# Performance work log

Hardware: AMD Instinct MI355X
Metric: run time of the kernel (lower is better)

Reference implementation:

```python
import jax, jax.numpy as jnp
import numpy as np

A = 4096      # alleles
RPA = 20      # mean reads per allele
R = A * RPA   # total reads per data source
C = 12        # input channels (pileup features)
L = 32        # read window length
D = 32        # hidden feature dim
NOUT = 2


def setup_inputs() -> dict:
    key = jax.random.key(0)
    k = jax.random.split(key, 8)
    # ragged read counts per allele (alternating 16/24, mean 20, sums to R)
    counts0 = np.tile(np.array([16, 24], dtype=np.int64), A // 2)
    counts1 = np.tile(np.array([24, 16], dtype=np.int64), A // 2)
    return {
        "tensors0": jax.random.normal(k[0], (R, C, L), dtype=jnp.float32),
        "tensors1": jax.random.normal(k[1], (R, C, L), dtype=jnp.float32),
        "W0": jax.random.normal(k[2], (D, C), dtype=jnp.float32) * 0.1,
        "b0": jnp.zeros((D,), dtype=jnp.float32),
        "W1": jax.random.normal(k[3], (D, C), dtype=jnp.float32) * 0.1,
        "b1": jnp.zeros((D,), dtype=jnp.float32),
        "W2": jax.random.normal(k[4], (NOUT, 2 * D), dtype=jnp.float32) * 0.1,
        "b2": jnp.zeros((NOUT,), dtype=jnp.float32),
        "numReadsPerAllele0": jnp.asarray(counts0),
        "numReadsPerAllele1": jnp.asarray(counts1),
        "numAllelesPerSite": jnp.full((A // 2,), 2, dtype=jnp.int64),
        "depthMultiplier0": jnp.asarray(counts0, dtype=jnp.float32),
        "depthMultiplier1": jnp.asarray(counts1, dtype=jnp.float32),
    }


def _frames(t, W, b):
    # pointwise read-feature extractor: [R,C,L] -> [R,D,L]
    return jax.nn.relu(jnp.einsum('rcl,dc->rdl', t, W) + b[None, :, None])


def reference(tensors0, tensors1, W0, b0, W1, b1, W2, b2,
              numReadsPerAllele0, numReadsPerAllele1,
              numAllelesPerSite, depthMultiplier0, depthMultiplier1):
    nA = numReadsPerAllele0.shape[0]
    nR = tensors0.shape[0]
    # segment ids replace torch.split + per-segment torch.sum (ragged segment-sum)
    seg0 = jnp.repeat(jnp.arange(nA), numReadsPerAllele0, total_repeat_length=nR)
    seg1 = jnp.repeat(jnp.arange(nA), numReadsPerAllele1, total_repeat_length=nR)

    frames0 = _frames(tensors0, W0, b0)  # [R,D,L]
    frames1 = _frames(tensors1, W1, b1)

    red0 = jax.ops.segment_sum(frames0, seg0, num_segments=nA)  # [A,D,L]
    red1 = jax.ops.segment_sum(frames1, seg1, num_segments=nA)

    # depth normalization (normalize() in the original)
    red0 = red0 / depthMultiplier0[:, None, None]
    red1 = red1 / depthMultiplier1[:, None, None]

    reduced = jnp.concatenate((red0, red1), axis=1)  # [A, 2D, L]

    # network2 (GraphSearcher): site-specific head modeled as pool + linear
    pooled = jnp.mean(reduced, axis=2)               # [A, 2D]
    return pooled @ W2.T + b2                        # [A, NOUT]
```

## Files before the change

kernel.cpp:

```cpp
#include <hip/hip_runtime.h>

#define A_ALLELES 4096
#define CCH 12
#define LW 32
#define DH 32
#define RDF (CCH * LW)

typedef __attribute__((ext_vector_type(8)))  short bf16x8;
typedef __attribute__((ext_vector_type(16))) float f32x16;

__device__ inline unsigned pk2(float fa, float fb) {
    const unsigned a = __float_as_uint(fa), b = __float_as_uint(fb);
    return ((a + 0x8000u) >> 16) | ((b + 0x8000u) & 0xffff0000u);
}

__global__ __launch_bounds__(256) void scan_kernel(
    const int* __restrict__ c0, const int* __restrict__ c1,
    int* __restrict__ o0, int* __restrict__ o1)
{
    const int* c = (blockIdx.x == 0) ? c0 : c1;
    int*       o = (blockIdx.x == 0) ? o0 : o1;

    __shared__ int part[256];
    const int tid  = threadIdx.x;
    const int base = tid * 16;

    int loc[16];
    int s = 0;
#pragma unroll
    for (int i = 0; i < 16; ++i) { loc[i] = c[base + i]; s += loc[i]; }
    part[tid] = s;
    __syncthreads();

    for (int st = 1; st < 256; st <<= 1) {
        int v = (tid >= st) ? part[tid - st] : 0;
        __syncthreads();
        part[tid] += v;
        __syncthreads();
    }

    int excl = (tid == 0) ? 0 : part[tid - 1];
#pragma unroll
    for (int i = 0; i < 16; ++i) { o[base + i] = excl; excl += loc[i]; }
}

__global__ __launch_bounds__(256, 4) void main_kernel(
    const float* __restrict__ t0, const float* __restrict__ t1,
    const float* __restrict__ W0, const float* __restrict__ b0,
    const float* __restrict__ W1, const float* __restrict__ b1,
    const float* __restrict__ W2, const float* __restrict__ b2,
    const int*  __restrict__ cnt0, const int* __restrict__ cnt1,
    const float* __restrict__ dm0, const float* __restrict__ dm1,
    const int*  __restrict__ offs0, const int* __restrict__ offs1,
    float* __restrict__ out)
{
    __shared__ float sW2[2 * 2 * DH];
    __shared__ float sB2[2];

    const int tid = threadIdx.x;
    if (tid < 2 * 2 * DH) sW2[tid] = W2[tid];
    if (tid < 2) sB2[tid] = b2[tid];
    __syncthreads();

    const int w    = tid >> 6;
    const int lane = tid & 63;
    const int src  = blockIdx.x >> 10;
    const int a    = ((blockIdx.x & 1023) << 2) | w;

    const float* __restrict__ tens = src ? t1 : t0;
    const int*   __restrict__ cnt  = src ? cnt1 : cnt0;
    const int*   __restrict__ offs = src ? offs1 : offs0;
    const float* __restrict__ dm   = src ? dm1 : dm0;
    const float* __restrict__ gW   = src ? W1 : W0;
    const float* __restrict__ gB   = src ? b1 : b0;

    const int l = lane & 31;
    const int h = lane >> 5;

    union { bf16x8 v; unsigned u[4]; } Af;
#pragma unroll
    for (int p = 0; p < 4; ++p) {
        const int c0 = h * 8 + 2 * p, c1 = c0 + 1;
        const float f0 = (c0 < CCH) ? gW[l * CCH + c0] : 0.f;
        const float f1 = (c1 < CCH) ? gW[l * CCH + c1] : 0.f;
        Af.u[p] = pk2(f0, f1);
    }
    f32x16 cb;
#pragma unroll
    for (int reg = 0; reg < 16; ++reg)
        cb[reg] = gB[(reg & 3) + 8 * (reg >> 2) + 4 * h];

    const int n     = cnt[a];
    const int start = offs[a];
    const float* rb = tens + (size_t)start * RDF;

    const int e    = lane & 1;
    const int jj   = (lane >> 1) & 15;
    const int half = lane >> 5;
    const int q0 = 2 * ((half * 8 + e)     * 16 + jj);
    const int q1 = 2 * ((half * 8 + 2 + e) * 16 + jj);
    const int q2 = 2 * ((4 + half * 2 + e) * 16 + jj);

    float acc[16];
#pragma unroll
    for (int r = 0; r < 16; ++r) acc[r] = 0.f;

#define LOADF2(A0, A1, A2, i) do {                                    \
        const float* _p = rb + (size_t)(i) * RDF;                     \
        A0 = *reinterpret_cast<const float2*>(_p + q0);               \
        A1 = *reinterpret_cast<const float2*>(_p + q1);               \
        A2 = *reinterpret_cast<const float2*>(_p + q2); } while (0)

#define CONSUMEF2(A0, A1, A2) do {                                    \
        const float p0x = __shfl_xor(A0.x, 1, 64);                    \
        const float p0y = __shfl_xor(A0.y, 1, 64);                    \
        const float p1x = __shfl_xor(A1.x, 1, 64);                    \
        const float p1y = __shfl_xor(A1.y, 1, 64);                    \
        const float p2x = __shfl_xor(A2.x, 1, 64);                    \
        const float p2y = __shfl_xor(A2.y, 1, 64);                    \
        const float c0v = e ? p0y : A0.x;     \
        const float c1v = e ? A0.y : p0x;    \
        const float c2v = e ? p1y : A1.x;    \
        const float c3v = e ? A1.y : p1x;    \
        const float vA  = e ? p2y : A2.x;    \
        const float vB  = e ? A2.y : p2x;    \
        const float vC  = __shfl_xor(vA, 32, 64);      \
        const float vD  = __shfl_xor(vB, 32, 64);      \
        union { bf16x8 v; unsigned u[4]; } Bf;                        \
        Bf.u[0] = pk2(c0v, c1v); Bf.u[1] = pk2(c2v, c3v);             \
        Bf.u[2] = pk2(vA, vB);   Bf.u[3] = pk2(vC, vD);               \
        const f32x16 Dv = __builtin_amdgcn_mfma_f32_32x32x16_bf16(    \
            Af.v, Bf.v, cb, 0, 0, 0);                                 \
        _Pragma("unroll")                                             \
        for (int r_ = 0; r_ < 16; ++r_) acc[r_] += fmaxf(Dv[r_], 0.f); } while (0)

    const int n2 = n & ~1;
    if (n2 >= 2) {
        float2 Ra0, Ra1, Ra2, Rb0, Rb1, Rb2;
        LOADF2(Ra0, Ra1, Ra2, 0);
        LOADF2(Rb0, Rb1, Rb2, 1);
        for (int i = 0; i + 4 <= n2; i += 2) {
            CONSUMEF2(Ra0, Ra1, Ra2); LOADF2(Ra0, Ra1, Ra2, i + 2);
            CONSUMEF2(Rb0, Rb1, Rb2); LOADF2(Rb0, Rb1, Rb2, i + 3);
        }
        CONSUMEF2(Ra0, Ra1, Ra2);
        CONSUMEF2(Rb0, Rb1, Rb2);
    }
    for (int i = n2; i < n; ++i) {
        float2 T0, T1, T2;
        LOADF2(T0, T1, T2, i);
        CONSUMEF2(T0, T1, T2);
    }
#undef LOADF2
#undef CONSUMEF2

#pragma unroll
    for (int r = 0; r < 16; ++r) {
#pragma unroll
        for (int mm = 1; mm < 32; mm <<= 1)
            acc[r] += __shfl_xor(acc[r], mm, 64);
    }

    const float scale = 1.f / (32.f * dm[a]);
    float c0s = 0.f, c1s = 0.f;
#pragma unroll
    for (int r = 0; r < 16; ++r) {
        const int d = (r & 3) + 8 * (r >> 2) + 4 * h;
        const float pv = acc[r] * scale;
        c0s = fmaf(pv, sW2[0 * 2 * DH + src * DH + d], c0s);
        c1s = fmaf(pv, sW2[1 * 2 * DH + src * DH + d], c1s);
    }
    c0s += __shfl_xor(c0s, 32, 64);
    c1s += __shfl_xor(c1s, 32, 64);

    if (lane == 0) {
        if (src == 0) { c0s += sB2[0]; c1s += sB2[1]; }
        atomicAdd(&out[a * 2 + 0], c0s);
        atomicAdd(&out[a * 2 + 1], c1s);
    }
}

extern "C" void kernel_launch(void* const* d_in, const int* in_sizes, int n_in,
                              void* d_out, int out_size, void* d_ws, size_t ws_size,
                              hipStream_t stream) {
    const float* t0  = (const float*)d_in[0];
    const float* t1  = (const float*)d_in[1];
    const float* W0  = (const float*)d_in[2];
    const float* b0  = (const float*)d_in[3];
    const float* W1  = (const float*)d_in[4];
    const float* b1  = (const float*)d_in[5];
    const float* W2  = (const float*)d_in[6];
    const float* b2  = (const float*)d_in[7];
    const int*  cnt0 = (const int*)d_in[8];
    const int*  cnt1 = (const int*)d_in[9];
    const float* dm0 = (const float*)d_in[11];
    const float* dm1 = (const float*)d_in[12];

    int* offs0 = (int*)d_ws;
    int* offs1 = offs0 + A_ALLELES;

    hipMemsetAsync(d_out, 0, (size_t)out_size * sizeof(float), stream);
    scan_kernel<<<2, 256, 0, stream>>>(cnt0, cnt1, offs0, offs1);

    main_kernel<<<2048, 256, 0, stream>>>(
        t0, t1, W0, b0, W1, b1, W2, b2,
        cnt0, cnt1, dm0, dm1, offs0, offs1, (float*)d_out);
}
```

Baseline: 298.2 us.

## Process four alleles per wave with a persistent loop and deeper prefetch

Each wave now loops over four (source, allele) work items instead of handling one, so the grid shrinks from 2048 to 512 blocks. The read prefetch ring grows from two reads in flight to four, and launch bounds relax from 4 to 2 waves-per-SIMD minimum to leave room for the extra registers. The aim is more memory-level parallelism per wave and less per-block launch overhead on this bandwidth-bound read stream. The cost is lower occupancy and possible load imbalance, since 512 blocks of 4 waves may not fill all CUs evenly.

```diff
diff --git a/kernel.cpp b/kernel.cpp
--- a/kernel.cpp
+++ b/kernel.cpp
@@ -44,7 +44,7 @@
     for (int i = 0; i < 16; ++i) { o[base + i] = excl; excl += loc[i]; }
 }
 
-__global__ __launch_bounds__(256, 4) void main_kernel(
+__global__ __launch_bounds__(256, 2) void main_kernel(
     const float* __restrict__ t0, const float* __restrict__ t1,
     const float* __restrict__ W0, const float* __restrict__ b0,
     const float* __restrict__ W1, const float* __restrict__ b1,
@@ -64,35 +64,10 @@
 
     const int w    = tid >> 6;
     const int lane = tid & 63;
-    const int src  = blockIdx.x >> 10;
-    const int a    = ((blockIdx.x & 1023) << 2) | w;
-
-    const float* __restrict__ tens = src ? t1 : t0;
-    const int*   __restrict__ cnt  = src ? cnt1 : cnt0;
-    const int*   __restrict__ offs = src ? offs1 : offs0;
-    const float* __restrict__ dm   = src ? dm1 : dm0;
-    const float* __restrict__ gW   = src ? W1 : W0;
-    const float* __restrict__ gB   = src ? b1 : b0;
+    const int g    = (blockIdx.x << 2) | w;
 
     const int l = lane & 31;
     const int h = lane >> 5;
-
-    union { bf16x8 v; unsigned u[4]; } Af;
-#pragma unroll
-    for (int p = 0; p < 4; ++p) {
-        const int c0 = h * 8 + 2 * p, c1 = c0 + 1;
-        const float f0 = (c0 < CCH) ? gW[l * CCH + c0] : 0.f;
-        const float f1 = (c1 < CCH) ? gW[l * CCH + c1] : 0.f;
-        Af.u[p] = pk2(f0, f1);
-    }
-    f32x16 cb;
-#pragma unroll
-    for (int reg = 0; reg < 16; ++reg)
-        cb[reg] = gB[(reg & 3) + 8 * (reg >> 2) + 4 * h];
-
-    const int n     = cnt[a];
-    const int start = offs[a];
-    const float* rb = tens + (size_t)start * RDF;
 
     const int e    = lane & 1;
     const int jj   = (lane >> 1) & 15;
@@ -101,9 +76,38 @@
     const int q1 = 2 * ((half * 8 + 2 + e) * 16 + jj);
     const int q2 = 2 * ((4 + half * 2 + e) * 16 + jj);
 
-    float acc[16];
-#pragma unroll
-    for (int r = 0; r < 16; ++r) acc[r] = 0.f;
+#pragma unroll 1
+    for (int k = 0; k < 4; ++k) {
+        const int src = k >> 1;
+        const int a   = g + ((k & 1) << 11);
+
+        const float* __restrict__ tens = src ? t1 : t0;
+        const int*   __restrict__ cnt  = src ? cnt1 : cnt0;
+        const int*   __restrict__ offs = src ? offs1 : offs0;
+        const float* __restrict__ dm   = src ? dm1 : dm0;
+        const float* __restrict__ gW   = src ? W1 : W0;
+        const float* __restrict__ gB   = src ? b1 : b0;
+
+        union { bf16x8 v; unsigned u[4]; } Af;
+#pragma unroll
+        for (int p = 0; p < 4; ++p) {
+            const int c0 = h * 8 + 2 * p, c1 = c0 + 1;
+            const float f0 = (c0 < CCH) ? gW[l * CCH + c0] : 0.f;
+            const float f1 = (c1 < CCH) ? gW[l * CCH + c1] : 0.f;
+            Af.u[p] = pk2(f0, f1);
+        }
+        f32x16 cb;
+#pragma unroll
+        for (int reg = 0; reg < 16; ++reg)
+            cb[reg] = gB[(reg & 3) + 8 * (reg >> 2) + 4 * h];
+
+        const int n     = cnt[a];
+        const int start = offs[a];
+        const float* rb = tens + (size_t)start * RDF;
+
+        float acc[16];
+#pragma unroll
+        for (int r = 0; r < 16; ++r) acc[r] = 0.f;
 
 #define LOADF2(A0, A1, A2, i) do {                                    \
         const float* _p = rb + (size_t)(i) * RDF;                     \
@@ -134,49 +138,56 @@
         _Pragma("unroll")                                             \
         for (int r_ = 0; r_ < 16; ++r_) acc[r_] += fmaxf(Dv[r_], 0.f); } while (0)
 
-    const int n2 = n & ~1;
-    if (n2 >= 2) {
-        float2 Ra0, Ra1, Ra2, Rb0, Rb1, Rb2;
-        LOADF2(Ra0, Ra1, Ra2, 0);
-        LOADF2(Rb0, Rb1, Rb2, 1);
-        for (int i = 0; i + 4 <= n2; i += 2) {
-            CONSUMEF2(Ra0, Ra1, Ra2); LOADF2(Ra0, Ra1, Ra2, i + 2);
-            CONSUMEF2(Rb0, Rb1, Rb2); LOADF2(Rb0, Rb1, Rb2, i + 3);
-        }
-        CONSUMEF2(Ra0, Ra1, Ra2);
-        CONSUMEF2(Rb0, Rb1, Rb2);
-    }
-    for (int i = n2; i < n; ++i) {
-        float2 T0, T1, T2;
-        LOADF2(T0, T1, T2, i);
-        CONSUMEF2(T0, T1, T2);
-    }
+        const int nf = n & ~3;
+        if (nf >= 4) {
+            float2 A0, A1, A2, B0, B1, B2, C0, C1, C2, D0, D1, D2;
+            LOADF2(A0, A1, A2, 0);
+            LOADF2(B0, B1, B2, 1);
+            LOADF2(C0, C1, C2, 2);
+            LOADF2(D0, D1, D2, 3);
+            for (int i = 0; i + 8 <= nf; i += 4) {
+                CONSUMEF2(A0, A1, A2); LOADF2(A0, A1, A2, i + 4);
+                CONSUMEF2(B0, B1, B2); LOADF2(B0, B1, B2, i + 5);
+                CONSUMEF2(C0, C1, C2); LOADF2(C0, C1, C2, i + 6);
+                CONSUMEF2(D0, D1, D2); LOADF2(D0, D1, D2, i + 7);
+            }
+            CONSUMEF2(A0, A1, A2);
+            CONSUMEF2(B0, B1, B2);
+            CONSUMEF2(C0, C1, C2);
+            CONSUMEF2(D0, D1, D2);
+        }
+        for (int i = nf; i < n; ++i) {
+            float2 T0, T1, T2;
+            LOADF2(T0, T1, T2, i);
+            CONSUMEF2(T0, T1, T2);
+        }
 #undef LOADF2
 #undef CONSUMEF2
 
 #pragma unroll
-    for (int r = 0; r < 16; ++r) {
-#pragma unroll
-        for (int mm = 1; mm < 32; mm <<= 1)
-            acc[r] += __shfl_xor(acc[r], mm, 64);
-    }
-
-    const float scale = 1.f / (32.f * dm[a]);
-    float c0s = 0.f, c1s = 0.f;
-#pragma unroll
-    for (int r = 0; r < 16; ++r) {
-        const int d = (r & 3) + 8 * (r >> 2) + 4 * h;
-        const float pv = acc[r] * scale;
-        c0s = fmaf(pv, sW2[0 * 2 * DH + src * DH + d], c0s);
-        c1s = fmaf(pv, sW2[1 * 2 * DH + src * DH + d], c1s);
-    }
-    c0s += __shfl_xor(c0s, 32, 64);
-    c1s += __shfl_xor(c1s, 32, 64);
-
-    if (lane == 0) {
-        if (src == 0) { c0s += sB2[0]; c1s += sB2[1]; }
-        atomicAdd(&out[a * 2 + 0], c0s);
-        atomicAdd(&out[a * 2 + 1], c1s);
+        for (int r = 0; r < 16; ++r) {
+#pragma unroll
+            for (int mm = 1; mm < 32; mm <<= 1)
+                acc[r] += __shfl_xor(acc[r], mm, 64);
+        }
+
+        const float scale = 1.f / (32.f * dm[a]);
+        float c0s = 0.f, c1s = 0.f;
+#pragma unroll
+        for (int r = 0; r < 16; ++r) {
+            const int d = (r & 3) + 8 * (r >> 2) + 4 * h;
+            const float pv = acc[r] * scale;
+            c0s = fmaf(pv, sW2[0 * 2 * DH + src * DH + d], c0s);
+            c1s = fmaf(pv, sW2[1 * 2 * DH + src * DH + d], c1s);
+        }
+        c0s += __shfl_xor(c0s, 32, 64);
+        c1s += __shfl_xor(c1s, 32, 64);
+
+        if (lane == 0) {
+            if (src == 0) { c0s += sB2[0]; c1s += sB2[1]; }
+            atomicAdd(&out[a * 2 + 0], c0s);
+            atomicAdd(&out[a * 2 + 1], c1s);
+        }
     }
 }
 
@@ -202,7 +213,7 @@
     hipMemsetAsync(d_out, 0, (size_t)out_size * sizeof(float), stream);
     scan_kernel<<<2, 256, 0, stream>>>(cnt0, cnt1, offs0, offs1);
 
-    main_kernel<<<2048, 256, 0, stream>>>(
+    main_kernel<<<512, 256, 0, stream>>>(
         t0, t1, W0, b0, W1, b1, W2, b2,
         cnt0, cnt1, dm0, dm1, offs0, offs1, (float*)d_out);
 }
```

Result: no change. 293.1 us (-1.7%).
